# Kernel tuning notes

Hardware: AMD Instinct MI355X
Metric: run time of the kernel (lower is better)

The kernel has to match this reference:

```python
import jax, jax.numpy as jnp
import numpy as np

NUM_HEADS = 12


def _qkv_split(x, qkv_w, num_heads):
    B, N, C = x.shape
    hd = C // num_heads
    qkv = (x @ qkv_w).reshape(B, N, 3, num_heads, hd)
    qkv = jnp.transpose(qkv, (2, 0, 3, 1, 4))  # [3, B, H, N, hd]
    return qkv[0], qkv[1], qkv[2]


def setup_inputs() -> dict:
    key = jax.random.key(0)
    k1, k2, k3, k4 = jax.random.split(key, 4)
    B, N, C = 8, 1024, 768
    s = 0.02
    return {
        "x1": jax.random.normal(k1, (B, N, C), dtype=jnp.float32),
        "x2": jax.random.normal(k2, (B, N, C), dtype=jnp.float32),
        "qkv_w": jax.random.normal(k3, (C, 3 * C), dtype=jnp.float32) * s,
        "proj_w": jax.random.normal(k4, (C, C), dtype=jnp.float32) * s,
        "proj_b": jnp.zeros((C,), dtype=jnp.float32),
    }


def reference(x1, x2, qkv_w, proj_w, proj_b):
    B, N, C = x1.shape
    H = NUM_HEADS
    hd = C // H
    scale = hd ** (-0.5)

    q, k, v = _qkv_split(x1, qkv_w, H)    # each [B, H, N, hd]
    q2, k2, v2 = _qkv_split(x2, qkv_w, H)

    # self-attention branch: q attends to k/v (from x1)
    attn1 = jax.nn.softmax(jnp.einsum('bhqd,bhkd->bhqk', q, k) * scale, axis=-1)
    o1 = jnp.einsum('bhqk,bhkd->bhqd', attn1, v)

    # cross-attention branch: same q attends to k2/v2 (from x2)
    attn2 = jax.nn.softmax(jnp.einsum('bhqd,bhkd->bhqk', q, k2) * scale, axis=-1)
    o2 = jnp.einsum('bhqk,bhkd->bhqd', attn2, v2)

    o1 = jnp.transpose(o1, (0, 2, 1, 3)).reshape(B, N, C) @ proj_w + proj_b
    o2 = jnp.transpose(o2, (0, 2, 1, 3)).reshape(B, N, C) @ proj_w + proj_b
    return (o1, o2)
```

## Files before the change

### kernel.cpp

```cpp
#include <hip/hip_runtime.h>
#include <hip/hip_bf16.h>

#define N_ 1024
#define C_ 768
#define H_ 12

typedef unsigned short u16;
typedef __attribute__((ext_vector_type(8))) short bf16x8;
typedef __attribute__((ext_vector_type(4))) float f32x4;
typedef __attribute__((ext_vector_type(16))) float f32x16;

#define MFMA16(a, b, c) __builtin_amdgcn_mfma_f32_16x16x32_bf16(a, b, c, 0, 0, 0)
#define MFMA32(a, b, c) __builtin_amdgcn_mfma_f32_32x32x16_bf16(a, b, c, 0, 0, 0)

#define GLDS16(gp, lp) __builtin_amdgcn_global_load_lds(                     \
    (const __attribute__((address_space(1))) void*)(gp),                     \
    (__attribute__((address_space(3))) void*)(lp), 16, 0, 0)

__device__ __forceinline__ u16 f2bu(float x) {
    unsigned u = __float_as_uint(x);
    unsigned r = (u + 0x7fffu + ((u >> 16) & 1u)) >> 16;
    return (u16)r;
}

__device__ __forceinline__ unsigned cvtpk(float a, float b) {
    unsigned d;
    asm("v_cvt_pk_bf16_f32 %0, %1, %2" : "=v"(d) : "v"(a), "v"(b));
    return d;
}

__global__ __launch_bounds__(256) void prep(
    const float* __restrict__ x1, const float* __restrict__ x2,
    const float* __restrict__ qkv_w, const float* __restrict__ proj_w,
    u16* __restrict__ d1, u16* __restrict__ d2,
    u16* __restrict__ wqkvT, u16* __restrict__ wprojT)
{
    const int bid = blockIdx.x;
    if (bid < 2304) {
        __shared__ float t[32][33];
        const int txi = bid % 96, ty = bid / 96;
        const bool isq = txi < 72;
        const float* W = isq ? qkv_w : proj_w;
        u16* WT = isq ? wqkvT : wprojT;
        const int CC = isq ? 2304 : 768;
        const int c0 = (isq ? txi : txi - 72) * 32;
        const int r0 = ty * 32;
        const int tx = threadIdx.x & 31, tyy = threadIdx.x >> 5;
#pragma unroll
        for (int i = 0; i < 4; ++i) {
            int r = tyy + i * 8;
            t[r][tx] = W[(size_t)(r0 + r) * CC + c0 + tx];
        }
        __syncthreads();
#pragma unroll
        for (int i = 0; i < 4; ++i) {
            int c = tyy + i * 8;
            WT[(size_t)(c0 + c) * 768 + r0 + tx] = f2bu(t[tx][c]);
        }
    } else {
        const size_t G = 786432;
        for (size_t i = (size_t)(bid - 2304) * 256 + threadIdx.x; i < 2 * G;
             i += (size_t)1536 * 256) {
            const float* src = (i < G) ? x1 : x2;
            u16* dst = (i < G) ? d1 : d2;
            size_t g = (i < G) ? i : i - G;
            float4 f0 = ((const float4*)src)[g * 2];
            float4 f1 = ((const float4*)src)[g * 2 + 1];
            ushort4 lo, hi;
            lo.x = f2bu(f0.x); lo.y = f2bu(f0.y); lo.z = f2bu(f0.z); lo.w = f2bu(f0.w);
            hi.x = f2bu(f1.x); hi.y = f2bu(f1.y); hi.z = f2bu(f1.z); hi.w = f2bu(f1.w);
            ((ushort4*)dst)[g * 2] = lo;
            ((ushort4*)dst)[g * 2 + 1] = hi;
        }
    }
}

__global__ __launch_bounds__(512) void qkv_gemm(
    const u16* __restrict__ A1, const u16* __restrict__ A2,
    const u16* __restrict__ BT, u16* __restrict__ qd,
    u16* __restrict__ k1d, u16* __restrict__ k2d,
    u16* __restrict__ vt1d, u16* __restrict__ vt2d)
{
    __shared__ u16 As[2][128 * 64];
    __shared__ u16 Bs[2][128 * 64];
    const int tid = threadIdx.x;
    const int w = tid >> 6, lane = tid & 63;
    const int c31 = lane & 31, h = lane >> 5;
    const int wm = w >> 2, wn = w & 3;
    const int id = blockIdx.x;
    const int xcd = id & 7, j = id >> 3;
    const int by = xcd * 8 + j / 30;
    const int bx = j % 30;
    const bool first = bx < 18;
    const u16* A = first ? A1 : A2;
    const int row0 = by * 128;
    const int nc0 = first ? bx * 128 : 768 + (bx - 18) * 128;

    f32x16 acc[2];
#pragma unroll
    for (int i = 0; i < 2; ++i)
#pragma unroll
        for (int e = 0; e < 16; ++e) acc[i][e] = 0.f;

    const int srow = tid >> 3;
    const int sch = ((tid & 7) ^ (srow & 7)) * 8;
    int aoff[2], boff[2];
#pragma unroll
    for (int i = 0; i < 2; ++i) {
        int row = i * 64 + srow;
        aoff[i] = (row0 + row) * C_ + sch;
        boff[i] = (nc0 + row) * C_ + sch;
    }
    char* adst0 = (char*)&As[0][0] + w * 1024;
    char* bdst0 = (char*)&Bs[0][0] + w * 1024;
    auto stage = [&](int buf, int k0) {
#pragma unroll
        for (int i = 0; i < 2; ++i) {
            GLDS16(A + aoff[i] + k0, adst0 + buf * 16384 + i * 8192);
            GLDS16(BT + boff[i] + k0, bdst0 + buf * 16384 + i * 8192);
        }
    };

    const int ra0 = wm * 64 + c31, ra1 = ra0 + 32;
    const int rb0 = wn * 32 + c31;

    stage(0, 0);
    for (int kt = 0; kt < 12; ++kt) {
        const int buf = kt & 1;
        if (kt < 11) {
            stage(buf ^ 1, (kt + 1) * 64);
            asm volatile("s_waitcnt vmcnt(4)" ::: "memory");
        } else {
            asm volatile("s_waitcnt vmcnt(0)" ::: "memory");
        }
        __builtin_amdgcn_s_barrier();
        const char* abase = (const char*)&As[0][0] + buf * 16384;
        const char* bbase = (const char*)&Bs[0][0] + buf * 16384;
        __builtin_amdgcn_s_setprio(1);
#pragma unroll
        for (int kh = 0; kh < 4; ++kh) {
            bf16x8 a0 = *(const bf16x8*)(abase + ra0 * 128 + (((2 * kh + h) ^ (ra0 & 7)) * 16));
            bf16x8 a1 = *(const bf16x8*)(abase + ra1 * 128 + (((2 * kh + h) ^ (ra1 & 7)) * 16));
            bf16x8 b0 = *(const bf16x8*)(bbase + rb0 * 128 + (((2 * kh + h) ^ (rb0 & 7)) * 16));
            acc[0] = MFMA32(a0, b0, acc[0]);
            acc[1] = MFMA32(a1, b0, acc[1]);
        }
        __builtin_amdgcn_s_setprio(0);
        asm volatile("" ::: "memory");
        __builtin_amdgcn_s_barrier();
    }

    u16* kd  = first ? k1d : k2d;
    u16* vtd = first ? vt1d : vt2d;
    const int col = nc0 + wn * 32 + c31;
    const int sec = col / C_;
    const int hh = (col % C_) >> 6;
    const int d = col & 63;
    const float scl = (sec == 0) ? 0.180336877f : 1.0f;
#pragma unroll
    for (int mt = 0; mt < 2; ++mt)
#pragma unroll
        for (int r = 0; r < 16; ++r) {
            int row = row0 + wm * 64 + mt * 32 + (r & 3) + 8 * (r >> 2) + 4 * h;
            int b = row >> 10, n = row & 1023;
            u16 val = f2bu(acc[mt][r] * scl);
            size_t bh = (size_t)(b * H_ + hh);
            if (sec == 0)      qd[(bh * N_ + n) * 64 + d] = val;
            else if (sec == 1) kd[(bh * N_ + n) * 64 + d] = val;
            else {
                int nprm = (n & ~63) | (((n & 15) << 2) | ((n >> 4) & 3));
                vtd[(bh * 64 + d) * N_ + nprm] = val;
            }
        }
}

__global__ __launch_bounds__(512) void proj_gemm(
    const u16* __restrict__ A1, const u16* __restrict__ A2,
    const u16* __restrict__ BT, const float* __restrict__ bias,
    float* __restrict__ out)
{
    __shared__ u16 As[2][128 * 64];
    __shared__ u16 Bs[2][128 * 64];
    const int tid = threadIdx.x;
    const int w = tid >> 6, lane = tid & 63;
    const int c31 = lane & 31, h = lane >> 5;
    const int wm = w >> 2, wn = w & 3;
    const int id = blockIdx.x;
    const int xcd = id & 7, j = id >> 3;
    const int byg = xcd * 16 + j / 6;
    const int sel = byg >> 6;
    const u16* A = sel ? A2 : A1;
    float* op = out + (size_t)sel * 8192 * C_;
    const int row0 = (byg & 63) * 128;
    const int nc0 = (j % 6) * 128;

    f32x16 acc[2];
#pragma unroll
    for (int i = 0; i < 2; ++i)
#pragma unroll
        for (int e = 0; e < 16; ++e) acc[i][e] = 0.f;

    const int srow = tid >> 3;
    const int sch = ((tid & 7) ^ (srow & 7)) * 8;
    int aoff[2], boff[2];
#pragma unroll
    for (int i = 0; i < 2; ++i) {
        int row = i * 64 + srow;
        aoff[i] = (row0 + row) * C_ + sch;
        boff[i] = (nc0 + row) * C_ + sch;
    }
    char* adst0 = (char*)&As[0][0] + w * 1024;
    char* bdst0 = (char*)&Bs[0][0] + w * 1024;
    auto stage = [&](int buf, int k0) {
#pragma unroll
        for (int i = 0; i < 2; ++i) {
            GLDS16(A + aoff[i] + k0, adst0 + buf * 16384 + i * 8192);
            GLDS16(BT + boff[i] + k0, bdst0 + buf * 16384 + i * 8192);
        }
    };

    const int ra0 = wm * 64 + c31, ra1 = ra0 + 32;
    const int rb0 = wn * 32 + c31;

    stage(0, 0);
    for (int kt = 0; kt < 12; ++kt) {
        const int buf = kt & 1;
        if (kt < 11) {
            stage(buf ^ 1, (kt + 1) * 64);
            asm volatile("s_waitcnt vmcnt(4)" ::: "memory");
        } else {
            asm volatile("s_waitcnt vmcnt(0)" ::: "memory");
        }
        __builtin_amdgcn_s_barrier();
        const char* abase = (const char*)&As[0][0] + buf * 16384;
        const char* bbase = (const char*)&Bs[0][0] + buf * 16384;
        __builtin_amdgcn_s_setprio(1);
#pragma unroll
        for (int kh = 0; kh < 4; ++kh) {
            bf16x8 a0 = *(const bf16x8*)(abase + ra0 * 128 + (((2 * kh + h) ^ (ra0 & 7)) * 16));
            bf16x8 a1 = *(const bf16x8*)(abase + ra1 * 128 + (((2 * kh + h) ^ (ra1 & 7)) * 16));
            bf16x8 b0 = *(const bf16x8*)(bbase + rb0 * 128 + (((2 * kh + h) ^ (rb0 & 7)) * 16));
            acc[0] = MFMA32(a0, b0, acc[0]);
            acc[1] = MFMA32(a1, b0, acc[1]);
        }
        __builtin_amdgcn_s_setprio(0);
        asm volatile("" ::: "memory");
        __builtin_amdgcn_s_barrier();
    }

    const int col = nc0 + wn * 32 + c31;
#pragma unroll
    for (int mt = 0; mt < 2; ++mt)
#pragma unroll
        for (int r = 0; r < 16; ++r) {
            int row = row0 + wm * 64 + mt * 32 + (r & 3) + 8 * (r >> 2) + 4 * h;
            op[(size_t)row * C_ + col] = acc[mt][r] + bias[col];
        }
}

__global__ __launch_bounds__(256) void attn_mfma(
    const u16* __restrict__ Q,
    const u16* __restrict__ K1, const u16* __restrict__ VT1,
    const u16* __restrict__ K2, const u16* __restrict__ VT2,
    u16* __restrict__ O1, u16* __restrict__ O2)
{
    __shared__ u16 Ks[2][64 * 64];
    __shared__ u16 Vs[2][64 * 64];
    __shared__ u16 Ps[4][32 * 72];
    const int tid = threadIdx.x;
    const int w = tid >> 6, lane = tid & 63;
    const int g = lane >> 4, ln = lane & 15;
    const int id = blockIdx.x;
    const int xcd = id & 7, j = id >> 3;
    const int unit = j >> 3;
    const int qb = j & 7;
    const int br = unit >= 12;
    const int bh = xcd * 12 + (br ? unit - 12 : unit);
    const int qw = qb * 128 + w * 32;
    const size_t hb = (size_t)bh * N_ * 64;

    const u16* Kb = (br ? K2 : K1) + hb;
    const u16* Vb = (br ? VT2 : VT1) + hb;
    const u16* Qb = Q + hb;
    u16* O        = br ? O2 : O1;

    bf16x8 qf[2][2];
#pragma unroll
    for (int mt = 0; mt < 2; ++mt)
#pragma unroll
        for (int s = 0; s < 2; ++s)
            qf[mt][s] = *(const bf16x8*)(Qb + (size_t)(qw + mt * 16 + ln) * 64 + s * 32 + g * 8);

    f32x4 o[2][4];
    float lsum[2][4];
#pragma unroll
    for (int mt = 0; mt < 2; ++mt) {
#pragma unroll
        for (int t = 0; t < 4; ++t) o[mt][t] = (f32x4){0.f, 0.f, 0.f, 0.f};
#pragma unroll
        for (int r = 0; r < 4; ++r) lsum[mt][r] = 0.f;
    }

    auto stage = [&](int buf, int key0) {
#pragma unroll
        for (int i = 0; i < 2; ++i) {
            int L = (i * 256 + tid) * 16;
            int row = L >> 7;
            int sw = (((L >> 4) & 7) ^ (row & 7)) * 8;
            GLDS16(Kb + (size_t)(key0 + row) * 64 + sw,
                   (char*)&Ks[buf][0] + i * 4096 + w * 1024);
            GLDS16(Vb + (size_t)row * N_ + key0 + sw,
                   (char*)&Vs[buf][0] + i * 4096 + w * 1024);
        }
    };

    u16* pw = &Ps[w][0];
    const int r7 = ln & 7;

    stage(0, 0);
    __syncthreads();
    for (int kt = 0; kt < 16; ++kt) {
        const int buf = kt & 1;
        if (kt < 15) stage(buf ^ 1, (kt + 1) * 64);
        const char* kbase = (const char*)&Ks[buf][0];
        f32x4 st[2][4];
        __builtin_amdgcn_s_setprio(1);
#pragma unroll
        for (int nt = 0; nt < 4; ++nt) {
            const char* krow = kbase + (nt * 16 + ln) * 128;
            bf16x8 kf0 = *(const bf16x8*)(krow + ((g ^ r7) * 16));
            bf16x8 kf1 = *(const bf16x8*)(krow + (((g + 4) ^ r7) * 16));
#pragma unroll
            for (int mt = 0; mt < 2; ++mt) {
                f32x4 z = (f32x4){0.f, 0.f, 0.f, 0.f};
                z = MFMA16(qf[mt][0], kf0, z);
                z = MFMA16(qf[mt][1], kf1, z);
                st[mt][nt] = z;
            }
        }
        __builtin_amdgcn_s_setprio(0);
#pragma unroll
        for (int mt = 0; mt < 2; ++mt)
#pragma unroll
            for (int r = 0; r < 4; ++r) {
                float p0 = __builtin_amdgcn_exp2f(st[mt][0][r]);
                float p1 = __builtin_amdgcn_exp2f(st[mt][1][r]);
                float p2 = __builtin_amdgcn_exp2f(st[mt][2][r]);
                float p3 = __builtin_amdgcn_exp2f(st[mt][3][r]);
                lsum[mt][r] += (p0 + p1) + (p2 + p3);
                uint2 pk;
                pk.x = cvtpk(p0, p1);
                pk.y = cvtpk(p2, p3);
                int prow = mt * 16 + g * 4 + r;
                *(uint2*)((char*)pw + prow * 144 + ln * 8) = pk;
            }
        const char* vbase = (const char*)&Vs[buf][0];
        __builtin_amdgcn_s_setprio(1);
#pragma unroll
        for (int s = 0; s < 2; ++s) {
            bf16x8 pa[2];
            pa[0] = *(const bf16x8*)((const char*)pw + (0 + ln) * 144 + s * 64 + g * 16);
            pa[1] = *(const bf16x8*)((const char*)pw + (16 + ln) * 144 + s * 64 + g * 16);
#pragma unroll
            for (int t = 0; t < 4; ++t) {
                bf16x8 vf = *(const bf16x8*)(vbase + (t * 16 + ln) * 128 + (((s * 4 + g) ^ r7) * 16));
#pragma unroll
                for (int mt = 0; mt < 2; ++mt) o[mt][t] = MFMA16(pa[mt], vf, o[mt][t]);
            }
        }
        __builtin_amdgcn_s_setprio(0);
        __syncthreads();
    }
    const int b = bh / H_, h = bh % H_;
#pragma unroll
    for (int mt = 0; mt < 2; ++mt)
#pragma unroll
        for (int r = 0; r < 4; ++r) {
            float ls = lsum[mt][r];
#pragma unroll
            for (int off = 8; off; off >>= 1) ls += __shfl_xor(ls, off);
            float inv = 1.f / ls;
            int n = qw + mt * 16 + g * 4 + r;
            u16* orow = O + ((size_t)(b * N_) + n) * C_ + h * 64 + ln;
#pragma unroll
            for (int t = 0; t < 4; ++t)
                orow[t * 16] = f2bu(o[mt][t][r] * inv);
        }
}

extern "C" void kernel_launch(void* const* d_in, const int* in_sizes, int n_in,
                              void* d_out, int out_size, void* d_ws, size_t ws_size,
                              hipStream_t stream) {
    const float* x1     = (const float*)d_in[0];
    const float* x2     = (const float*)d_in[1];
    const float* qkv_w  = (const float*)d_in[2];
    const float* proj_w = (const float*)d_in[3];
    const float* proj_b = (const float*)d_in[4];
    float* out = (float*)d_out;

    u16* ws = (u16*)d_ws;
    const size_t SZ = (size_t)8 * H_ * N_ * 64;
    u16* wqkvT  = ws;
    u16* wprojT = wqkvT + (size_t)2304 * 768;
    u16* q      = wprojT + (size_t)768 * 768;
    u16* k1     = q + SZ;
    u16* vT1    = k1 + SZ;
    u16* slotA  = vT1 + SZ;
    u16* vT2    = slotA + SZ;
    u16* slotB  = vT2 + SZ;
    u16* x1c = slotA, *o2p = slotA;
    u16* x2c = slotB, *o1p = slotB;
    u16* k2buf = (u16*)(out + SZ);

    prep<<<3840, 256, 0, stream>>>(x1, x2, qkv_w, proj_w, x1c, x2c, wqkvT, wprojT);
    qkv_gemm<<<1920, 512, 0, stream>>>(x1c, x2c, wqkvT, q, k1, k2buf, vT1, vT2);
    attn_mfma<<<1536, 256, 0, stream>>>(q, k1, vT1, k2buf, vT2, o1p, o2p);
    proj_gemm<<<768, 512, 0, stream>>>(o1p, o2p, wprojT, proj_b, out);
}
```

Before: 210.0 us.

## Enlarge QKV GEMM tiles to 256x256 with finer-grained staged pipeline

The QKV projection GEMM now computes 256x256 output tiles per block instead of 128x128, so the grid shrinks from 1920 to 480 blocks. Each wave holds a 4x2 set of 32x32 accumulators, which raises operand reuse from LDS and cuts global traffic per FLOP. Global-to-LDS loads are split into quarter-stages interleaved with the per-k MFMA steps across a double buffer. The change also drops the setprio hints in proj_gemm. Costs are higher register and LDS use (64KB) and fewer blocks, which can lower occupancy and load balance across the CUs.

```diff
diff --git a/kernel.cpp b/kernel.cpp
--- a/kernel.cpp
+++ b/kernel.cpp
@@ -81,95 +81,114 @@
     u16* __restrict__ k1d, u16* __restrict__ k2d,
     u16* __restrict__ vt1d, u16* __restrict__ vt2d)
 {
-    __shared__ u16 As[2][128 * 64];
-    __shared__ u16 Bs[2][128 * 64];
+    __shared__ u16 As[2][2][8192];
+    __shared__ u16 Bs[2][2][8192];
     const int tid = threadIdx.x;
     const int w = tid >> 6, lane = tid & 63;
     const int c31 = lane & 31, h = lane >> 5;
     const int wm = w >> 2, wn = w & 3;
     const int id = blockIdx.x;
     const int xcd = id & 7, j = id >> 3;
-    const int by = xcd * 8 + j / 30;
-    const int bx = j % 30;
-    const bool first = bx < 18;
-    const u16* A = first ? A1 : A2;
-    const int row0 = by * 128;
-    const int nc0 = first ? bx * 128 : 768 + (bx - 18) * 128;
-
-    f32x16 acc[2];
-#pragma unroll
-    for (int i = 0; i < 2; ++i)
-#pragma unroll
-        for (int e = 0; e < 16; ++e) acc[i][e] = 0.f;
-
-    const int srow = tid >> 3;
-    const int sch = ((tid & 7) ^ (srow & 7)) * 8;
-    int aoff[2], boff[2];
-#pragma unroll
-    for (int i = 0; i < 2; ++i) {
-        int row = i * 64 + srow;
-        aoff[i] = (row0 + row) * C_ + sch;
-        boff[i] = (nc0 + row) * C_ + sch;
-    }
-    char* adst0 = (char*)&As[0][0] + w * 1024;
-    char* bdst0 = (char*)&Bs[0][0] + w * 1024;
-    auto stage = [&](int buf, int k0) {
-#pragma unroll
-        for (int i = 0; i < 2; ++i) {
-            GLDS16(A + aoff[i] + k0, adst0 + buf * 16384 + i * 8192);
-            GLDS16(BT + boff[i] + k0, bdst0 + buf * 16384 + i * 8192);
+    const int by = xcd * 4 + j / 15;
+    const int bx = j % 15;
+    const bool first = bx < 9;
+    const u16* Ain = first ? A1 : A2;
+    const int row0 = by * 256;
+    const int bcol0 = first ? bx * 256 : 768 + (bx - 9) * 256;
+
+    f32x16 acc[4][2];
+#pragma unroll
+    for (int i = 0; i < 4; ++i)
+#pragma unroll
+        for (int jj = 0; jj < 2; ++jj)
+#pragma unroll
+            for (int e = 0; e < 16; ++e) acc[i][jj][e] = 0.f;
+
+    const int r0t = tid >> 3;
+    const int csrc = ((tid & 7) ^ (r0t & 7)) * 8;
+    const u16* srcA = Ain + (size_t)(row0 + r0t) * 768 + csrc;
+    const u16* srcB = BT + (size_t)(bcol0 + r0t) * 768 + csrc;
+    char* dstA = (char*)As + w * 1024;
+    char* dstB = (char*)Bs + w * 1024;
+
+    auto stage = [&](int ts, int part) {
+        const int d = ts & 1, hf = part & 1;
+        const int lb = (d * 2 + hf) << 14;
+        const int go = hf * 98304 + ts * 64;
+        if (part < 2) {
+            GLDS16(srcA + go,         dstA + lb);
+            GLDS16(srcA + go + 49152, dstA + lb + 8192);
+        } else {
+            GLDS16(srcB + go,         dstB + lb);
+            GLDS16(srcB + go + 49152, dstB + lb + 8192);
         }
     };
 
-    const int ra0 = wm * 64 + c31, ra1 = ra0 + 32;
-    const int rb0 = wn * 32 + c31;
-
-    stage(0, 0);
-    for (int kt = 0; kt < 12; ++kt) {
-        const int buf = kt & 1;
-        if (kt < 11) {
-            stage(buf ^ 1, (kt + 1) * 64);
-            asm volatile("s_waitcnt vmcnt(4)" ::: "memory");
-        } else {
-            asm volatile("s_waitcnt vmcnt(0)" ::: "memory");
-        }
-        __builtin_amdgcn_s_barrier();
-        const char* abase = (const char*)&As[0][0] + buf * 16384;
-        const char* bbase = (const char*)&Bs[0][0] + buf * 16384;
-        __builtin_amdgcn_s_setprio(1);
-#pragma unroll
-        for (int kh = 0; kh < 4; ++kh) {
-            bf16x8 a0 = *(const bf16x8*)(abase + ra0 * 128 + (((2 * kh + h) ^ (ra0 & 7)) * 16));
-            bf16x8 a1 = *(const bf16x8*)(abase + ra1 * 128 + (((2 * kh + h) ^ (ra1 & 7)) * 16));
-            bf16x8 b0 = *(const bf16x8*)(bbase + rb0 * 128 + (((2 * kh + h) ^ (rb0 & 7)) * 16));
-            acc[0] = MFMA32(a0, b0, acc[0]);
-            acc[1] = MFMA32(a1, b0, acc[1]);
-        }
-        __builtin_amdgcn_s_setprio(0);
-        asm volatile("" ::: "memory");
-        __builtin_amdgcn_s_barrier();
+    stage(0, 0); stage(0, 1); stage(0, 2); stage(0, 3);
+
+    for (int it = 0; it < 6; ++it) {
+#pragma unroll
+        for (int p = 0; p < 8; ++p) {
+            const int d = p >> 2;
+            const int kh = p & 3;
+            const int ts = 2 * it + 1 + d;
+            if (ts < 12) stage(ts, p & 3);
+            if (p == 0) {
+                asm volatile("s_waitcnt vmcnt(2)" ::: "memory");
+                __builtin_amdgcn_s_barrier();
+            } else if (p == 4) {
+                if (it < 5) asm volatile("s_waitcnt vmcnt(2)" ::: "memory");
+                else        asm volatile("s_waitcnt vmcnt(0)" ::: "memory");
+                __builtin_amdgcn_s_barrier();
+            }
+            const char* ab = (const char*)As + ((d * 2 + wm) << 14);
+            const char* bb = (const char*)Bs + ((d * 2 + (wn >> 1)) << 14);
+            bf16x8 af[4], bfr[2];
+#pragma unroll
+            for (int mt = 0; mt < 4; ++mt) {
+                int ar = mt * 32 + c31;
+                af[mt] = *(const bf16x8*)(ab + ar * 128 + (((kh * 2 + h) ^ (ar & 7)) * 16));
+            }
+#pragma unroll
+            for (int nt = 0; nt < 2; ++nt) {
+                int br = (wn & 1) * 64 + nt * 32 + c31;
+                bfr[nt] = *(const bf16x8*)(bb + br * 128 + (((kh * 2 + h) ^ (br & 7)) * 16));
+            }
+            __builtin_amdgcn_s_setprio(1);
+#pragma unroll
+            for (int mt = 0; mt < 4; ++mt)
+#pragma unroll
+                for (int nt = 0; nt < 2; ++nt)
+                    acc[mt][nt] = MFMA32(af[mt], bfr[nt], acc[mt][nt]);
+            __builtin_amdgcn_s_setprio(0);
+            asm volatile("" ::: "memory");
+            __builtin_amdgcn_s_barrier();
+        }
     }
 
     u16* kd  = first ? k1d : k2d;
     u16* vtd = first ? vt1d : vt2d;
-    const int col = nc0 + wn * 32 + c31;
-    const int sec = col / C_;
-    const int hh = (col % C_) >> 6;
-    const int d = col & 63;
-    const float scl = (sec == 0) ? 0.180336877f : 1.0f;
-#pragma unroll
-    for (int mt = 0; mt < 2; ++mt)
-#pragma unroll
-        for (int r = 0; r < 16; ++r) {
-            int row = row0 + wm * 64 + mt * 32 + (r & 3) + 8 * (r >> 2) + 4 * h;
-            int b = row >> 10, n = row & 1023;
-            u16 val = f2bu(acc[mt][r] * scl);
-            size_t bh = (size_t)(b * H_ + hh);
-            if (sec == 0)      qd[(bh * N_ + n) * 64 + d] = val;
-            else if (sec == 1) kd[(bh * N_ + n) * 64 + d] = val;
-            else {
-                int nprm = (n & ~63) | (((n & 15) << 2) | ((n >> 4) & 3));
-                vtd[(bh * 64 + d) * N_ + nprm] = val;
+#pragma unroll
+    for (int mt = 0; mt < 4; ++mt)
+#pragma unroll
+        for (int nt = 0; nt < 2; ++nt) {
+            const int col = bcol0 + wn * 64 + nt * 32 + c31;
+            const int sec = col / C_;
+            const int hh = (col % C_) >> 6;
+            const int dd = col & 63;
+            const float scl = (sec == 0) ? 0.180336877f : 1.0f;
+#pragma unroll
+            for (int r = 0; r < 16; ++r) {
+                int row = row0 + wm * 128 + mt * 32 + (r & 3) + 8 * (r >> 2) + 4 * h;
+                int b = row >> 10, n = row & 1023;
+                u16 val = f2bu(acc[mt][nt][r] * scl);
+                size_t bh = (size_t)(b * H_ + hh);
+                if (sec == 0)      qd[(bh * N_ + n) * 64 + dd] = val;
+                else if (sec == 1) kd[(bh * N_ + n) * 64 + dd] = val;
+                else {
+                    int nprm = (n & ~63) | (((n & 15) << 2) | ((n >> 4) & 3));
+                    vtd[(bh * 64 + dd) * N_ + nprm] = val;
+                }
             }
         }
 }
@@ -234,7 +253,6 @@
         __builtin_amdgcn_s_barrier();
         const char* abase = (const char*)&As[0][0] + buf * 16384;
         const char* bbase = (const char*)&Bs[0][0] + buf * 16384;
-        __builtin_amdgcn_s_setprio(1);
 #pragma unroll
         for (int kh = 0; kh < 4; ++kh) {
             bf16x8 a0 = *(const bf16x8*)(abase + ra0 * 128 + (((2 * kh + h) ^ (ra0 & 7)) * 16));
@@ -243,7 +261,6 @@
             acc[0] = MFMA32(a0, b0, acc[0]);
             acc[1] = MFMA32(a1, b0, acc[1]);
         }
-        __builtin_amdgcn_s_setprio(0);
         asm volatile("" ::: "memory");
         __builtin_amdgcn_s_barrier();
     }
@@ -413,7 +430,7 @@
     u16* k2buf = (u16*)(out + SZ);
 
     prep<<<3840, 256, 0, stream>>>(x1, x2, qkv_w, proj_w, x1c, x2c, wqkvT, wprojT);
-    qkv_gemm<<<1920, 512, 0, stream>>>(x1c, x2c, wqkvT, q, k1, k2buf, vT1, vT2);
+    qkv_gemm<<<480, 512, 0, stream>>>(x1c, x2c, wqkvT, q, k1, k2buf, vT1, vT2);
     attn_mfma<<<1536, 256, 0, stream>>>(q, k1, vT1, k2buf, vT2, o1p, o2p);
     proj_gemm<<<768, 512, 0, stream>>>(o1p, o2p, wprojT, proj_b, out);
 }
```

After: 231.5 us. 1.1x slower.
